# Kernel optimization log

Hardware: AMD Instinct MI355X
Metric: run time of the kernel (lower is better)

The kernel has to match this reference:

```python
import jax, jax.numpy as jnp
import numpy as np

B, C, T = 128, 16, 16384
WINDOW_RATIO = 0.25
W = int(np.ceil(WINDOW_RATIO * T))  # warp_size = 4096
LMAX = T + W                        # max warped length (scale=2 case)
SCALES = (0.5, 2.0)


def setup_inputs() -> dict:
    key = jax.random.key(0)
    k1, k2, k3 = jax.random.split(key, 3)
    x = jax.random.normal(k1, (B, C, T), dtype=jnp.float32)
    # np.random.randint(low=1, high=T - W - 1)
    window_starts = jax.random.randint(k2, (B,), 1, T - W - 1).astype(jnp.int32)
    # per-sample scale choice from {0.5, 2.0}; new_len = int(W * scale)
    pick = jax.random.bernoulli(k3, 0.5, (B,))
    new_len = jnp.where(pick, int(W * SCALES[1]), int(W * SCALES[0])).astype(jnp.int32)
    return {"x": x, "window_starts": window_starts, "new_len": new_len}


def _warp_sample(xc, s, nl):
    """Window-warp one sample. xc: (C, T); s, nl: scalar int32.

    Stage 1 builds the (padded) 'warped' signal of true length L = T + nl - W:
      [0, s)        -> original samples
      [s, s+nl)     -> window resampled from W to nl points (np.interp)
      [s+nl, L)     -> original tail samples
    Every warped[j] is a linear interp of xc at a fractional source position,
    so we compute positions then gather+lerp (exactly np.interp with xp=arange).
    Stage 2 resamples warped (length L) back to T points (second np.interp).
    """
    j = jnp.arange(LMAX, dtype=jnp.float32)
    sf = s.astype(jnp.float32)
    nlf = nl.astype(jnp.float32)
    in_win = (j >= sf) & (j < sf + nlf)
    after = j >= sf + nlf
    # source position in the original time axis for each warped index j
    pos = jnp.where(
        in_win,
        sf + (j - sf) * (W - 1.0) / jnp.maximum(nlf - 1.0, 1.0),
        jnp.where(after, j - nlf + W, j),
    )
    pos = jnp.clip(pos, 0.0, T - 1.0)
    lo = jnp.floor(pos).astype(jnp.int32)
    hi = jnp.minimum(lo + 1, T - 1)
    f = pos - lo
    warped = xc[:, lo] * (1.0 - f) + xc[:, hi] * f  # (C, LMAX); entries past L unused

    L_i = T + nl - W  # true warped length (traced int)
    Lf = L_i.astype(jnp.float32)
    # np.interp(arange(T), linspace(0, T-1, L), warped): query index = t*(L-1)/(T-1)
    q = jnp.arange(T, dtype=jnp.float32) * (Lf - 1.0) / (T - 1.0)
    qlo = jnp.floor(q).astype(jnp.int32)
    qhi = jnp.minimum(qlo + 1, L_i - 1)
    qf = q - qlo
    return warped[:, qlo] * (1.0 - qf) + warped[:, qhi] * qf  # (C, T)


def reference(x, window_starts, new_len):
    # x: (B, C, T) -> module transposes to (B, T, C), warps per sample/channel,
    # transposes back; equivalent to operating on (C, T) directly per sample.
    return jax.vmap(_warp_sample)(x, window_starts, new_len)
```

## Files before the change

### kernel.cpp

```cpp
#include <hip/hip_runtime.h>

#define NB 128
#define NC 16
#define NT 16384
#define NW 4096

__global__ __launch_bounds__(256) void rww_kernel(
    const float* __restrict__ x,
    const int* __restrict__ window_starts,
    const int* __restrict__ new_len,
    float* __restrict__ out)
{
    const int b = blockIdx.y;
    const int t = blockIdx.x * 256 + threadIdx.x;

    const int s  = window_starts[b];
    const int nl = new_len[b];
    const float sf  = (float)s;
    const float nlf = (float)nl;
    const int   L   = NT + nl - NW;
    const float Lf  = (float)L;

    float qpos = (float)t * (Lf - 1.0f) / (float)(NT - 1);
    int   qlo  = (int)floorf(qpos);
    int   qhi  = min(qlo + 1, L - 1);
    float qf   = qpos - (float)qlo;
    const float gq = 1.0f - qf;

    const float* xb = x   + (size_t)b * NC * NT;
    float*       ob = out + (size_t)b * NC * NT;

    if (qhi < s) {
        #pragma unroll
        for (int c = 0; c < NC; ++c) {
            const float* xc = xb + c * NT;
            float r = xc[qlo] * gq + xc[qhi] * qf;
            __builtin_nontemporal_store(r, ob + c * NT + t);
        }
        return;
    }
    if ((float)qlo >= sf + nlf) {
        const int off = NW - nl;
        #pragma unroll
        for (int c = 0; c < NC; ++c) {
            const float* xc = xb + c * NT;
            float r = xc[qlo + off] * gq + xc[qhi + off] * qf;
            __builtin_nontemporal_store(r, ob + c * NT + t);
        }
        return;
    }

    const float den = fmaxf(nlf - 1.0f, 1.0f);
    int lo0, hi0, lo1, hi1;
    float f0, f1;
    {
        float jf = (float)qlo;
        float pos;
        if (jf >= sf + nlf)      pos = jf - nlf + (float)NW;
        else if (jf >= sf)       pos = sf + (jf - sf) * (float)(NW - 1) / den;
        else                     pos = jf;
        pos = fminf(fmaxf(pos, 0.0f), (float)(NT - 1));
        lo0 = (int)floorf(pos);
        hi0 = min(lo0 + 1, NT - 1);
        f0  = pos - (float)lo0;
    }
    {
        float jf = (float)qhi;
        float pos;
        if (jf >= sf + nlf)      pos = jf - nlf + (float)NW;
        else if (jf >= sf)       pos = sf + (jf - sf) * (float)(NW - 1) / den;
        else                     pos = jf;
        pos = fminf(fmaxf(pos, 0.0f), (float)(NT - 1));
        lo1 = (int)floorf(pos);
        hi1 = min(lo1 + 1, NT - 1);
        f1  = pos - (float)lo1;
    }

    const float g0 = 1.0f - f0;
    const float g1 = 1.0f - f1;

    #pragma unroll
    for (int c = 0; c < NC; ++c) {
        const float* xc = xb + c * NT;
        float v0 = xc[lo0] * g0 + xc[hi0] * f0;
        float v1 = xc[lo1] * g1 + xc[hi1] * f1;
        __builtin_nontemporal_store(v0 * gq + v1 * qf, ob + c * NT + t);
    }
}

extern "C" void kernel_launch(void* const* d_in, const int* in_sizes, int n_in,
                              void* d_out, int out_size, void* d_ws, size_t ws_size,
                              hipStream_t stream) {
    const float* x   = (const float*)d_in[0];
    const int*   ws  = (const int*)d_in[1];
    const int*   nl  = (const int*)d_in[2];
    float*       out = (float*)d_out;

    dim3 grid(NT / 256, NB);
    dim3 block(256);
    rww_kernel<<<grid, block, 0, stream>>>(x, ws, nl, out);
}
```

Before: 49.38 us.

## Stage source window in LDS and emit vectorized float4 stores

Each block computes the source-index range its 256 output samples need and loads that span for all 16 channels into shared memory with float4 reads. Each thread then produces 4 consecutive outputs for 4 channels, doing the gathers from LDS and writing one float4 per channel. This replaces scattered, partly redundant global gathers with coalesced vector loads and wider stores. It adds a __syncthreads and LDS traffic, and clamps the span to 512 floats, which is only enough for the 2x-compression region at these sizes.

```diff
diff --git a/kernel.cpp b/kernel.cpp
--- a/kernel.cpp
+++ b/kernel.cpp
@@ -4,6 +4,10 @@
 #define NC 16
 #define NT 16384
 #define NW 4096
+#define TPB 256
+#define SPANROW 512
+
+typedef float f32x4 __attribute__((ext_vector_type(4)));
 
 __global__ __launch_bounds__(256) void rww_kernel(
     const float* __restrict__ x,
@@ -11,80 +15,108 @@
     const int* __restrict__ new_len,
     float* __restrict__ out)
 {
-    const int b = blockIdx.y;
-    const int t = blockIdx.x * 256 + threadIdx.x;
+    __shared__ float lds[NC][SPANROW];
+
+    const int b   = blockIdx.y;
+    const int t0  = blockIdx.x * TPB;
+    const int tid = threadIdx.x;
 
     const int s  = window_starts[b];
     const int nl = new_len[b];
     const float sf  = (float)s;
     const float nlf = (float)nl;
+    const float den = fmaxf(nlf - 1.0f, 1.0f);
     const int   L   = NT + nl - NW;
     const float Lf  = (float)L;
 
-    float qpos = (float)t * (Lf - 1.0f) / (float)(NT - 1);
-    int   qlo  = (int)floorf(qpos);
-    int   qhi  = min(qlo + 1, L - 1);
-    float qf   = qpos - (float)qlo;
-    const float gq = 1.0f - qf;
-
-    const float* xb = x   + (size_t)b * NC * NT;
-    float*       ob = out + (size_t)b * NC * NT;
-
-    if (qhi < s) {
-        #pragma unroll
-        for (int c = 0; c < NC; ++c) {
-            const float* xc = xb + c * NT;
-            float r = xc[qlo] * gq + xc[qhi] * qf;
-            __builtin_nontemporal_store(r, ob + c * NT + t);
-        }
-        return;
-    }
-    if ((float)qlo >= sf + nlf) {
-        const int off = NW - nl;
-        #pragma unroll
-        for (int c = 0; c < NC; ++c) {
-            const float* xc = xb + c * NT;
-            float r = xc[qlo + off] * gq + xc[qhi + off] * qf;
-            __builtin_nontemporal_store(r, ob + c * NT + t);
-        }
-        return;
-    }
-
-    const float den = fmaxf(nlf - 1.0f, 1.0f);
-    int lo0, hi0, lo1, hi1;
-    float f0, f1;
-    {
-        float jf = (float)qlo;
+    auto pos_of = [&](int j) -> float {
+        float jf = (float)j;
         float pos;
         if (jf >= sf + nlf)      pos = jf - nlf + (float)NW;
         else if (jf >= sf)       pos = sf + (jf - sf) * (float)(NW - 1) / den;
         else                     pos = jf;
-        pos = fminf(fmaxf(pos, 0.0f), (float)(NT - 1));
-        lo0 = (int)floorf(pos);
-        hi0 = min(lo0 + 1, NT - 1);
-        f0  = pos - (float)lo0;
-    }
+        return fminf(fmaxf(pos, 0.0f), (float)(NT - 1));
+    };
+
+    int winstart, span;
     {
-        float jf = (float)qhi;
-        float pos;
-        if (jf >= sf + nlf)      pos = jf - nlf + (float)NW;
-        else if (jf >= sf)       pos = sf + (jf - sf) * (float)(NW - 1) / den;
-        else                     pos = jf;
-        pos = fminf(fmaxf(pos, 0.0f), (float)(NT - 1));
-        lo1 = (int)floorf(pos);
-        hi1 = min(lo1 + 1, NT - 1);
-        f1  = pos - (float)lo1;
+        float qp0 = (float)t0 * (Lf - 1.0f) / (float)(NT - 1);
+        int   jlo = (int)floorf(qp0);
+        float qpm = (float)(t0 + TPB - 1) * (Lf - 1.0f) / (float)(NT - 1);
+        int   jhi = min((int)floorf(qpm) + 1, L - 1);
+        float pmin = pos_of(jlo);
+        float pmax = pos_of(jhi);
+        winstart = ((int)floorf(pmin)) & ~3;
+        if (winstart < 0) winstart = 0;
+        int need_end = min((int)floorf(pmax) + 2, NT);
+        span = (need_end - winstart + 3) & ~3;
+        if (span > SPANROW) span = SPANROW;
+        if (winstart + span > NT) winstart = NT - span;
     }
 
-    const float g0 = 1.0f - f0;
-    const float g1 = 1.0f - f1;
+    const float* xb = x + (size_t)b * NC * NT;
+    const int nv = span >> 2;
+    #pragma unroll
+    for (int it = 0; it < 8; ++it) {
+        int idx  = it * TPB + tid;
+        int c    = idx >> 7;
+        int col4 = idx & 127;
+        if (col4 < nv) {
+            f32x4 v = *(const f32x4*)(xb + c * NT + winstart + col4 * 4);
+            *(f32x4*)&lds[c][col4 * 4] = v;
+        }
+    }
+    __syncthreads();
 
+    const int tq = tid & 63;
+    const int c0 = (tid >> 6) * 4;
+
+    float g0a[4], f0a[4], g1a[4], f1a[4], gqa[4], qfa[4];
+    int   r0l[4], r0h[4], r1l[4], r1h[4];
     #pragma unroll
-    for (int c = 0; c < NC; ++c) {
-        const float* xc = xb + c * NT;
-        float v0 = xc[lo0] * g0 + xc[hi0] * f0;
-        float v1 = xc[lo1] * g1 + xc[hi1] * f1;
-        __builtin_nontemporal_store(v0 * gq + v1 * qf, ob + c * NT + t);
+    for (int i = 0; i < 4; ++i) {
+        const int t = t0 + tq * 4 + i;
+        float qpos = (float)t * (Lf - 1.0f) / (float)(NT - 1);
+        int   qlo  = (int)floorf(qpos);
+        int   qhi  = min(qlo + 1, L - 1);
+        float qf   = qpos - (float)qlo;
+
+        float p0 = pos_of(qlo);
+        int lo0 = (int)floorf(p0);
+        int hi0 = min(lo0 + 1, NT - 1);
+        f0a[i] = p0 - (float)lo0;
+        g0a[i] = 1.0f - f0a[i];
+        r0l[i] = lo0 - winstart;
+        r0h[i] = hi0 - winstart;
+
+        float p1 = pos_of(qhi);
+        int lo1 = (int)floorf(p1);
+        int hi1 = min(lo1 + 1, NT - 1);
+        f1a[i] = p1 - (float)lo1;
+        g1a[i] = 1.0f - f1a[i];
+        r1l[i] = lo1 - winstart;
+        r1h[i] = hi1 - winstart;
+
+        qfa[i] = qf;
+        gqa[i] = 1.0f - qf;
+    }
+
+    float* ob = out + (size_t)b * NC * NT + t0 + tq * 4;
+    #pragma unroll
+    for (int cc = 0; cc < 4; ++cc) {
+        const int c = c0 + cc;
+        f32x4 r;
+        #pragma unroll
+        for (int i = 0; i < 4; ++i) {
+            float a0 = lds[c][r0l[i]];
+            float b0 = lds[c][r0h[i]];
+            float a1 = lds[c][r1l[i]];
+            float b1 = lds[c][r1h[i]];
+            float v0 = a0 * g0a[i] + b0 * f0a[i];
+            float v1 = a1 * g1a[i] + b1 * f1a[i];
+            r[i] = v0 * gqa[i] + v1 * qfa[i];
+        }
+        __builtin_nontemporal_store(r, (f32x4*)(ob + c * NT));
     }
 }
 
@@ -96,7 +128,7 @@
     const int*   nl  = (const int*)d_in[2];
     float*       out = (float*)d_out;
 
-    dim3 grid(NT / 256, NB);
-    dim3 block(256);
+    dim3 grid(NT / TPB, NB);
+    dim3 block(TPB);
     rww_kernel<<<grid, block, 0, stream>>>(x, ws, nl, out);
 }
```

After: 47.29 us. -4.3%, faster.
